# Optimization experiments

Measured on AMD Instinct MI355X. Metric: run time of the kernel, lower is better.

Reference implementation:

```python
import jax, jax.numpy as jnp
import numpy as np

EMBED_DIM = 512
NUM_HEADS = 8
HEAD_DIM = EMBED_DIM // NUM_HEADS  # 64


def setup_inputs() -> dict:
    key = jax.random.key(0)
    ks = jax.random.split(key, 11)
    B, S, E, dh = 4, 2048, EMBED_DIM, HEAD_DIM
    s_small = 1.0 / np.sqrt(dh)
    s_big = 1.0 / np.sqrt(E)
    return {
        "Q": jax.random.normal(ks[0], (B, S, E), jnp.float32),
        "K": jax.random.normal(ks[1], (B, S, E), jnp.float32),
        "V": jax.random.normal(ks[2], (B, S, E), jnp.float32),
        "Wq_w": jax.random.normal(ks[3], (dh, dh), jnp.float32) * s_small,
        "Wq_b": jnp.zeros((dh,), jnp.float32),
        "Wk_w": jax.random.normal(ks[4], (dh, dh), jnp.float32) * s_small,
        "Wk_b": jnp.zeros((dh,), jnp.float32),
        "Wv_w": jax.random.normal(ks[5], (dh, dh), jnp.float32) * s_small,
        "Wv_b": jnp.zeros((dh,), jnp.float32),
        "Wo_w": jax.random.normal(ks[6], (E, E), jnp.float32) * s_big,
        "Wo_b": jnp.zeros((E,), jnp.float32),
    }


def reference(Q, K, V, Wq_w, Wq_b, Wk_w, Wk_b, Wv_w, Wv_b, Wo_w, Wo_b):
    B, S, E = Q.shape
    H, dh = NUM_HEADS, HEAD_DIM
    # split heads: [B,S,E] -> [B,S,H,dh]; per-head shared linear (torch y = x @ W.T + b)
    q = jnp.einsum('bshd,od->bsho', Q.reshape(B, S, H, dh), Wq_w) + Wq_b
    k = jnp.einsum('bshd,od->bsho', K.reshape(B, S, H, dh), Wk_w) + Wk_b
    v = jnp.einsum('bshd,od->bsho', V.reshape(B, S, H, dh), Wv_w) + Wv_b
    # [B,H,S,dh]
    q = q.transpose(0, 2, 1, 3)
    k = k.transpose(0, 2, 1, 3)
    v = v.transpose(0, 2, 1, 3)
    scores = jnp.einsum('bhqd,bhkd->bhqk', q, k) / np.sqrt(dh)  # full N x N scores (faithful to naive impl)
    probs = jax.nn.softmax(scores, axis=-1)
    attn = jnp.einsum('bhqk,bhkd->bhqd', probs, v)
    # combine heads: [B,H,S,dh] -> [B,S,E]
    out = attn.transpose(0, 2, 1, 3).reshape(B, S, E)
    return out @ Wo_w.T + Wo_b
```

## Files before the change

### kernel.cpp

```cpp
#include <hip/hip_runtime.h>

typedef float  f32x4  __attribute__((ext_vector_type(4)));
typedef float  f32x16 __attribute__((ext_vector_type(16)));
typedef short  s16x8  __attribute__((ext_vector_type(8)));

constexpr int Bn = 4, Sn = 2048, En = 512, Hn = 8;
constexpr int BH = Bn * Hn;
constexpr int NT = Sn / 64;
constexpr float QSCL = 0.125f * 1.44269504088896f;

static __device__ __forceinline__ ushort f2bf(float f) {
  union { float f; uint u; } v; v.f = f;
  uint r = v.u + 0x7fffu + ((v.u >> 16) & 1u);
  return (ushort)(r >> 16);
}
static __device__ __forceinline__ float hexp2(float x) {
  float r; asm("v_exp_f32 %0, %1" : "=v"(r) : "v"(x)); return r;
}
static __device__ __forceinline__ uint pkbf(float lo, float hi2) {
  uint r; asm("v_cvt_pk_bf16_f32 %0, %1, %2" : "=v"(r) : "v"(lo), "v"(hi2)); return r;
}
static __device__ __forceinline__ uint2 pack4(float a, float b, float c, float d) {
  uint2 u; u.x = pkbf(a, b); u.y = pkbf(c, d); return u;
}
#define SWAP32(a, b) asm("v_permlane32_swap_b32 %0, %1" : "+v"(a), "+v"(b))
static __device__ __forceinline__ s16x8 mk8(uint a, uint b, uint c, uint d) {
  union { uint u[4]; s16x8 v; } x; x.u[0] = a; x.u[1] = b; x.u[2] = c; x.u[3] = d; return x.v;
}
#define MFMA32(A, B, C) __builtin_amdgcn_mfma_f32_32x32x16_bf16((A), (B), (C), 0, 0, 0)
#define MFMA16(A, B, C) __builtin_amdgcn_mfma_f32_16x16x32_bf16((A), (B), (C), 0, 0, 0)
#define GLDS(SRC, DST) __builtin_amdgcn_global_load_lds( \
    (const __attribute__((address_space(1))) void*)(SRC), \
    (__attribute__((address_space(3))) void*)(DST), 16, 0, 0)

__global__ __launch_bounds__(256) void proj_kernel(
    const float* __restrict__ Qi, const float* __restrict__ Ki, const float* __restrict__ Vi,
    const float* __restrict__ Wq, const float* __restrict__ bq,
    const float* __restrict__ Wk, const float* __restrict__ bk,
    const float* __restrict__ Wv, const float* __restrict__ bv,
    ushort* __restrict__ qo, ushort* __restrict__ ko, ushort* __restrict__ vto)
{
  constexpr int LP = 72;
  __shared__ ushort Xl[64 * LP];
  __shared__ ushort Wl[64 * LP];
  const int role = blockIdx.z;
  const float* X    = role == 0 ? Qi : (role == 1 ? Ki : Vi);
  const float* W    = role == 0 ? Wq : (role == 1 ? Wk : Wv);
  const float* bias = role == 0 ? bq : (role == 1 ? bk : bv);
  const float oscl  = role == 0 ? QSCL : 1.0f;
  const int t = threadIdx.x, lane = t & 63, w = t >> 6;
  const int g = lane >> 4, ql = lane & 15;
  const int bh = blockIdx.y, b = bh >> 3, h = bh & 7;
  const int s0 = blockIdx.x * 64;

  {
    const int row = t >> 4, c = t & 15;
#pragma unroll
    for (int p = 0; p < 4; ++p) {
      const int rr = row + p * 16;
      const float4 wv = *(const float4*)(W + rr * 64 + c * 4);
      *(uint2*)&Wl[rr * LP + c * 4] = pack4(wv.x, wv.y, wv.z, wv.w);
      const float4 xv = *(const float4*)(X + ((size_t)b * Sn + s0 + rr) * En + h * 64 + c * 4);
      *(uint2*)&Xl[rr * LP + c * 4] = pack4(xv.x, xv.y, xv.z, xv.w);
    }
  }
  __syncthreads();

  f32x4 acc[4];
#pragma unroll
  for (int i = 0; i < 4; ++i) acc[i] = (f32x4){0.f, 0.f, 0.f, 0.f};
#pragma unroll
  for (int kc = 0; kc < 2; ++kc) {
    const s16x8 bfrag = *(const s16x8*)&Xl[(w * 16 + ql) * LP + kc * 32 + g * 8];
#pragma unroll
    for (int nt = 0; nt < 4; ++nt) {
      const s16x8 afrag = *(const s16x8*)&Wl[(nt * 16 + ql) * LP + kc * 32 + g * 8];
      acc[nt] = MFMA16(afrag, bfrag, acc[nt]);
    }
  }

  __syncthreads();
  const int sl = w * 16 + ql;
  if (role < 2) {
#pragma unroll
    for (int nt = 0; nt < 4; ++nt) {
      const int ob = nt * 16 + g * 4;
      *(uint2*)&Xl[sl * LP + ob] = pack4((acc[nt][0] + bias[ob]) * oscl,
                                         (acc[nt][1] + bias[ob + 1]) * oscl,
                                         (acc[nt][2] + bias[ob + 2]) * oscl,
                                         (acc[nt][3] + bias[ob + 3]) * oscl);
    }
    __syncthreads();
    ushort* dst = (role == 0 ? qo : ko) + (size_t)bh * Sn * 64;
    const int ro = t >> 3, ch = t & 7;
#pragma unroll
    for (int p = 0; p < 2; ++p) {
      const int row = ro + p * 32;
      const uint4 v = *(const uint4*)&Xl[row * LP + ch * 8];
      *(uint4*)&dst[(size_t)(s0 + row) * 64 + ch * 8] = v;
    }
  } else {
#pragma unroll
    for (int nt = 0; nt < 4; ++nt)
#pragma unroll
      for (int r = 0; r < 4; ++r) {
        const int o = nt * 16 + g * 4 + r;
        Xl[o * LP + sl] = f2bf(acc[nt][r] + bias[o]);
      }
    __syncthreads();
    const int ro = t >> 3, ch = t & 7;
#pragma unroll
    for (int p = 0; p < 2; ++p) {
      const int row = ro + p * 32;
      const uint4 v = *(const uint4*)&Xl[row * LP + ch * 8];
      *(uint4*)&vto[((size_t)bh * 64 + row) * Sn + s0 + ch * 8] = v;
    }
  }
}

__global__ __launch_bounds__(512, 4) void flash_kernel(
    const ushort* __restrict__ q, const ushort* __restrict__ k,
    const ushort* __restrict__ vt, ushort* __restrict__ attn)
{
  __shared__ __align__(16) char smem[36864];
  float* mrg = (float*)smem;
  const int tid = threadIdx.x, lane = tid & 63, w = tid >> 6;
  const int m = lane & 31, hi = lane >> 5;
  const int wl = w & 3, h2 = w >> 2;
  const int hx  = hi ^ (m & 7);
  const int hxv = hx ^ (h2 << 2);

  int lid = blockIdx.x + (blockIdx.y << 4);
  lid = (lid & 7) * 64 + (lid >> 3);
  const int bq = lid & 15, bh = lid >> 4;
  const int qrow = bq * 128 + wl * 32 + m;
  const int b = bh >> 3, h = bh & 7;

  const ushort* qp = q + ((size_t)bh * Sn + qrow) * 64 + hi * 8;
  const s16x8 qf0 = *(const s16x8*)(qp + 0);
  const s16x8 qf1 = *(const s16x8*)(qp + 16);
  const s16x8 qf2 = *(const s16x8*)(qp + 32);
  const s16x8 qf3 = *(const s16x8*)(qp + 48);

  const int srow = tid >> 3, sc = tid & 7, scs = sc ^ (srow & 7);
  const ushort* kS = k  + (size_t)bh * Sn * 64 + (size_t)srow * 64 + scs * 8;
  const ushort* vS = vt + ((size_t)bh * 64 + srow) * Sn + scs * 8;
  const uint dO = (uint)(tid * 16);
  char* KB0 = smem;          char* KB1 = smem + 8192;
  char* VB0 = smem + 16384;  char* VB1 = smem + 24576;

  const f32x16 z16 = {};
  f32x16 acc0 = {}, acc1 = {}, asum = {};
  union { ushort us[8]; s16x8 v; } onesU;
#pragma unroll
  for (int i = 0; i < 8; ++i) onesU.us[i] = 0x3F80;
  const s16x8 ones = onesU.v;

  GLDS(kS, KB0 + dO); GLDS(vS, VB0 + dO);
  kS += 4096; vS += 64;

#define LDK(KB, S)     (*(const s16x8*)((KB)  + ((h2 * 32 + m) * 64 + (((2 * (S)) ^ hx ) << 3)) * 2))
#define LDV(VB, DT, S) (*(const s16x8*)((VB)  + (((DT) * 32 + m) * 64 + (((2 * (S)) ^ hxv) << 3)) * 2))

#define STEP(T, KB, VB, KBn, VBn) do {                                      \
    if ((T) < NT - 1) {                                                     \
      GLDS(kS, (KBn) + dO); GLDS(vS, (VBn) + dO);                           \
      kS += 4096; vS += 64;                                                 \
      asm volatile("s_waitcnt vmcnt(2)" ::: "memory");                      \
    } else {                                                                \
      asm volatile("s_waitcnt vmcnt(0)" ::: "memory");                      \
    }                                                                       \
    __builtin_amdgcn_s_barrier();                                           \
    __builtin_amdgcn_sched_barrier(0);                                      \
    f32x16 sta, stb;                                                        \
    __builtin_amdgcn_s_setprio(1);                                          \
    sta = MFMA32(LDK(KB, 0), qf0, z16);                                     \
    sta = MFMA32(LDK(KB, 1), qf1, sta);                                     \
    stb = MFMA32(LDK(KB, 2), qf2, z16);                                     \
    stb = MFMA32(LDK(KB, 3), qf3, stb);                                     \
    __builtin_amdgcn_s_setprio(0);                                          \
    f32x16 p;                                                               \
    _Pragma("unroll")                                                       \
    for (int i = 0; i < 16; ++i) p[i] = hexp2(sta[i] + stb[i]);             \
    uint uA, uB, uC, uD, uE, uF, uG, uH;                                    \
    uA = pkbf(p[0], p[1]);   uB = pkbf(p[4], p[5]);   SWAP32(uA, uB);       \
    uC = pkbf(p[2], p[3]);   uD = pkbf(p[6], p[7]);   SWAP32(uC, uD);       \
    uE = pkbf(p[8], p[9]);   uF = pkbf(p[12], p[13]); SWAP32(uE, uF);       \
    uG = pkbf(p[10], p[11]); uH = pkbf(p[14], p[15]); SWAP32(uG, uH);       \
    const s16x8 pb0 = mk8(uA, uC, uB, uD);                                  \
    const s16x8 pb1 = mk8(uE, uG, uF, uH);                                  \
    __builtin_amdgcn_s_setprio(1);                                          \
    acc0 = MFMA32(LDV(VB, 0, 0), pb0, acc0);                                \
    acc0 = MFMA32(LDV(VB, 0, 1), pb1, acc0);                                \
    acc1 = MFMA32(LDV(VB, 1, 0), pb0, acc1);                                \
    acc1 = MFMA32(LDV(VB, 1, 1), pb1, acc1);                                \
    asum = MFMA32(ones, pb0, asum);                                         \
    asum = MFMA32(ones, pb1, asum);                                         \
    __builtin_amdgcn_s_setprio(0);                                          \
    __builtin_amdgcn_s_barrier();                                           \
    __builtin_amdgcn_sched_barrier(0);                                      \
  } while (0)

  for (int T = 0; T < NT; T += 2) {
    STEP(T,     KB0, VB0, KB1, VB1);
    STEP(T + 1, KB1, VB1, KB0, VB0);
  }
#undef STEP
#undef LDK
#undef LDV

  const float lT = asum[0];
  float* mp = mrg + (size_t)(wl * 64 + lane) * 36;
  __syncthreads();
  if (h2) {
#pragma unroll
    for (int i = 0; i < 4; ++i) {
      f32x4 t0 = {acc0[4 * i], acc0[4 * i + 1], acc0[4 * i + 2], acc0[4 * i + 3]};
      f32x4 t1 = {acc1[4 * i], acc1[4 * i + 1], acc1[4 * i + 2], acc1[4 * i + 3]};
      *(f32x4*)(mp + 4 * i) = t0;
      *(f32x4*)(mp + 16 + 4 * i) = t1;
    }
    mp[32] = lT;
  }
  __syncthreads();
  if (!h2) {
    const float inv = 1.0f / (lT + mp[32]);
    ushort* ap = attn + ((size_t)(b * Sn + qrow)) * En + h * 64;
#pragma unroll
    for (int g2 = 0; g2 < 4; ++g2) {
      float a0 = (acc0[g2 * 4 + 0] + mp[g2 * 4 + 0]) * inv;
      float a1 = (acc0[g2 * 4 + 1] + mp[g2 * 4 + 1]) * inv;
      float a2 = (acc0[g2 * 4 + 2] + mp[g2 * 4 + 2]) * inv;
      float a3 = (acc0[g2 * 4 + 3] + mp[g2 * 4 + 3]) * inv;
      float c0 = (acc1[g2 * 4 + 0] + mp[16 + g2 * 4 + 0]) * inv;
      float c1 = (acc1[g2 * 4 + 1] + mp[16 + g2 * 4 + 1]) * inv;
      float c2 = (acc1[g2 * 4 + 2] + mp[16 + g2 * 4 + 2]) * inv;
      float c3 = (acc1[g2 * 4 + 3] + mp[16 + g2 * 4 + 3]) * inv;
      uint2 u0, u1;
      u0.x = pkbf(a0, a1); u0.y = pkbf(a2, a3);
      u1.x = pkbf(c0, c1); u1.y = pkbf(c2, c3);
      *(uint2*)&ap[g2 * 8 + hi * 4]      = u0;
      *(uint2*)&ap[32 + g2 * 8 + hi * 4] = u1;
    }
  }
}

__global__ __launch_bounds__(512) void outproj_kernel(
    const ushort* __restrict__ attn, const float* __restrict__ Wo,
    const float* __restrict__ bo, float* __restrict__ out)
{
  constexpr int LP = 72;
  __shared__ ushort Al[128 * LP];
  __shared__ ushort Wl[64 * LP];
  const int t = threadIdx.x, lane = t & 63, w = t >> 6;
  const int g = lane >> 4, ml = lane & 15;
  const int wm = w & 3, wn = w >> 2;
  const int m0 = blockIdx.x * 128, n0 = blockIdx.y * 64;
  f32x4 acc[2][2];
#pragma unroll
  for (int i = 0; i < 2; ++i)
#pragma unroll
    for (int j = 0; j < 2; ++j) acc[i][j] = (f32x4){0.f, 0.f, 0.f, 0.f};

  const int arow = t >> 2, ac0 = t & 3;
  const int wrow = t >> 3, wc0 = t & 7;
  for (int e0 = 0; e0 < En; e0 += 64) {
    __syncthreads();
#pragma unroll
    for (int p = 0; p < 2; ++p) {
      const int c = ac0 + p * 4;
      const uint4 v = *(const uint4*)(attn + ((size_t)(m0 + arow)) * En + e0 + c * 8);
      *(uint4*)&Al[arow * LP + c * 8] = v;
    }
#pragma unroll
    for (int p = 0; p < 2; ++p) {
      const int c = wc0 + p * 8;
      const float4 v = *(const float4*)(Wo + ((size_t)(n0 + wrow)) * En + e0 + c * 4);
      *(uint2*)&Wl[wrow * LP + c * 4] = pack4(v.x, v.y, v.z, v.w);
    }
    __syncthreads();
#pragma unroll
    for (int kc = 0; kc < 2; ++kc) {
      s16x8 bfr[2];
#pragma unroll
      for (int mf = 0; mf < 2; ++mf)
        bfr[mf] = *(const s16x8*)&Al[(wm * 32 + mf * 16 + ml) * LP + kc * 32 + g * 8];
#pragma unroll
      for (int nf = 0; nf < 2; ++nf) {
        const s16x8 afr = *(const s16x8*)&Wl[(wn * 32 + nf * 16 + ml) * LP + kc * 32 + g * 8];
#pragma unroll
        for (int mf = 0; mf < 2; ++mf)
          acc[mf][nf] = MFMA16(afr, bfr[mf], acc[mf][nf]);
      }
    }
  }
#pragma unroll
  for (int mf = 0; mf < 2; ++mf) {
    const int mrow = m0 + wm * 32 + mf * 16 + ml;
#pragma unroll
    for (int nf = 0; nf < 2; ++nf) {
      const int ncol = n0 + wn * 32 + nf * 16 + g * 4;
      const float4 bias = *(const float4*)(bo + ncol);
      float4 o;
      o.x = acc[mf][nf][0] + bias.x;
      o.y = acc[mf][nf][1] + bias.y;
      o.z = acc[mf][nf][2] + bias.z;
      o.w = acc[mf][nf][3] + bias.w;
      *(float4*)&out[(size_t)mrow * En + ncol] = o;
    }
  }
}

extern "C" void kernel_launch(void* const* d_in, const int* in_sizes, int n_in,
                              void* d_out, int out_size, void* d_ws, size_t ws_size,
                              hipStream_t stream) {
  const float* Qi = (const float*)d_in[0];
  const float* Ki = (const float*)d_in[1];
  const float* Vi = (const float*)d_in[2];
  const float* Wq = (const float*)d_in[3];
  const float* bq = (const float*)d_in[4];
  const float* Wk = (const float*)d_in[5];
  const float* bk = (const float*)d_in[6];
  const float* Wv = (const float*)d_in[7];
  const float* bv = (const float*)d_in[8];
  const float* Wo = (const float*)d_in[9];
  const float* bo = (const float*)d_in[10];

  const size_t TEN = (size_t)BH * Sn * 64;
  ushort* qw  = (ushort*)d_ws;
  ushort* kw  = qw + TEN;
  ushort* vtw = kw + TEN;
  ushort* at  = vtw + TEN;

  proj_kernel<<<dim3(Sn / 64, BH, 3), 256, 0, stream>>>(
      Qi, Ki, Vi, Wq, bq, Wk, bk, Wv, bv, qw, kw, vtw);
  flash_kernel<<<dim3(16, 32), 512, 0, stream>>>(qw, kw, vtw, at);
  outproj_kernel<<<dim3(Bn * Sn / 128, En / 64), 512, 0, stream>>>(
      at, Wo, bo, (float*)d_out);
}
```

Before: 76.48 us.

## Split KV sequence across two blocks and merge partials in output projection

Adds an optional two-way split of the key/value sequence in the flash kernel, so each block handles half the KV tiles and writes unnormalized bf16 partial outputs plus row sums. The output-projection kernel then adds the two partials, divides by the summed normalizers and packs the result to bf16 before the GEMM. The goal is more blocks and better load balance across CUs. The cost is twice the intermediate traffic, an extra bf16 rounding of the partials, and more combine work in the outproj loads. The split only turns on when the workspace is large enough.

```diff
diff --git a/kernel.cpp b/kernel.cpp
--- a/kernel.cpp
+++ b/kernel.cpp
@@ -7,12 +7,16 @@
 constexpr int Bn = 4, Sn = 2048, En = 512, Hn = 8;
 constexpr int BH = Bn * Hn;
 constexpr int NT = Sn / 64;
+constexpr int TENc = BH * Sn * 64;
 constexpr float QSCL = 0.125f * 1.44269504088896f;
 
 static __device__ __forceinline__ ushort f2bf(float f) {
   union { float f; uint u; } v; v.f = f;
   uint r = v.u + 0x7fffu + ((v.u >> 16) & 1u);
   return (ushort)(r >> 16);
+}
+static __device__ __forceinline__ float bf2f(uint u16) {
+  union { uint i; float f; } v; v.i = u16 << 16; return v.f;
 }
 static __device__ __forceinline__ float hexp2(float x) {
   float r; asm("v_exp_f32 %0, %1" : "=v"(r) : "v"(x)); return r;
@@ -120,7 +124,7 @@
 
 __global__ __launch_bounds__(512, 4) void flash_kernel(
     const ushort* __restrict__ q, const ushort* __restrict__ k,
-    const ushort* __restrict__ vt, ushort* __restrict__ attn)
+    const ushort* __restrict__ vt, ushort* __restrict__ accP, float* __restrict__ lP)
 {
   __shared__ __align__(16) char smem[36864];
   float* mrg = (float*)smem;
@@ -130,6 +134,10 @@
   const int hx  = hi ^ (m & 7);
   const int hxv = hx ^ (h2 << 2);
 
+  const int nz = (int)gridDim.z;
+  const int nsteps = (nz == 2) ? (NT / 2) : NT;
+  const int kvoff = (nz == 2) ? (int)blockIdx.z * (Sn / 2) : 0;
+
   int lid = blockIdx.x + (blockIdx.y << 4);
   lid = (lid & 7) * 64 + (lid >> 3);
   const int bq = lid & 15, bh = lid >> 4;
@@ -143,8 +151,8 @@
   const s16x8 qf3 = *(const s16x8*)(qp + 48);
 
   const int srow = tid >> 3, sc = tid & 7, scs = sc ^ (srow & 7);
-  const ushort* kS = k  + (size_t)bh * Sn * 64 + (size_t)srow * 64 + scs * 8;
-  const ushort* vS = vt + ((size_t)bh * 64 + srow) * Sn + scs * 8;
+  const ushort* kS = k  + (size_t)bh * Sn * 64 + (size_t)(kvoff + srow) * 64 + scs * 8;
+  const ushort* vS = vt + ((size_t)bh * 64 + srow) * Sn + kvoff + scs * 8;
   const uint dO = (uint)(tid * 16);
   char* KB0 = smem;          char* KB1 = smem + 8192;
   char* VB0 = smem + 16384;  char* VB1 = smem + 24576;
@@ -163,7 +171,7 @@
 #define LDV(VB, DT, S) (*(const s16x8*)((VB)  + (((DT) * 32 + m) * 64 + (((2 * (S)) ^ hxv) << 3)) * 2))
 
 #define STEP(T, KB, VB, KBn, VBn) do {                                      \
-    if ((T) < NT - 1) {                                                     \
+    if ((T) < nsteps - 1) {                                                 \
       GLDS(kS, (KBn) + dO); GLDS(vS, (VBn) + dO);                           \
       kS += 4096; vS += 64;                                                 \
       asm volatile("s_waitcnt vmcnt(2)" ::: "memory");                      \
@@ -201,7 +209,7 @@
     __builtin_amdgcn_sched_barrier(0);                                      \
   } while (0)
 
-  for (int T = 0; T < NT; T += 2) {
+  for (int T = 0; T < nsteps; T += 2) {
     STEP(T,     KB0, VB0, KB1, VB1);
     STEP(T + 1, KB1, VB1, KB0, VB0);
   }
@@ -224,18 +232,21 @@
   }
   __syncthreads();
   if (!h2) {
-    const float inv = 1.0f / (lT + mp[32]);
-    ushort* ap = attn + ((size_t)(b * Sn + qrow)) * En + h * 64;
+    const float lTot = lT + mp[32];
+    const float sc = (nz == 1) ? (1.0f / lTot) : 1.0f;
+    if (nz == 2 && hi == 0)
+      lP[((size_t)blockIdx.z * (Bn * Sn) + b * Sn + qrow) * Hn + h] = lTot;
+    ushort* ap = accP + ((size_t)blockIdx.z * TENc) + ((size_t)(b * Sn + qrow)) * En + h * 64;
 #pragma unroll
     for (int g2 = 0; g2 < 4; ++g2) {
-      float a0 = (acc0[g2 * 4 + 0] + mp[g2 * 4 + 0]) * inv;
-      float a1 = (acc0[g2 * 4 + 1] + mp[g2 * 4 + 1]) * inv;
-      float a2 = (acc0[g2 * 4 + 2] + mp[g2 * 4 + 2]) * inv;
-      float a3 = (acc0[g2 * 4 + 3] + mp[g2 * 4 + 3]) * inv;
-      float c0 = (acc1[g2 * 4 + 0] + mp[16 + g2 * 4 + 0]) * inv;
-      float c1 = (acc1[g2 * 4 + 1] + mp[16 + g2 * 4 + 1]) * inv;
-      float c2 = (acc1[g2 * 4 + 2] + mp[16 + g2 * 4 + 2]) * inv;
-      float c3 = (acc1[g2 * 4 + 3] + mp[16 + g2 * 4 + 3]) * inv;
+      float a0 = (acc0[g2 * 4 + 0] + mp[g2 * 4 + 0]) * sc;
+      float a1 = (acc0[g2 * 4 + 1] + mp[g2 * 4 + 1]) * sc;
+      float a2 = (acc0[g2 * 4 + 2] + mp[g2 * 4 + 2]) * sc;
+      float a3 = (acc0[g2 * 4 + 3] + mp[g2 * 4 + 3]) * sc;
+      float c0 = (acc1[g2 * 4 + 0] + mp[16 + g2 * 4 + 0]) * sc;
+      float c1 = (acc1[g2 * 4 + 1] + mp[16 + g2 * 4 + 1]) * sc;
+      float c2 = (acc1[g2 * 4 + 2] + mp[16 + g2 * 4 + 2]) * sc;
+      float c3 = (acc1[g2 * 4 + 3] + mp[16 + g2 * 4 + 3]) * sc;
       uint2 u0, u1;
       u0.x = pkbf(a0, a1); u0.y = pkbf(a2, a3);
       u1.x = pkbf(c0, c1); u1.y = pkbf(c2, c3);
@@ -246,8 +257,8 @@
 }
 
 __global__ __launch_bounds__(512) void outproj_kernel(
-    const ushort* __restrict__ attn, const float* __restrict__ Wo,
-    const float* __restrict__ bo, float* __restrict__ out)
+    const ushort* __restrict__ accP, const float* __restrict__ lP, const int nz,
+    const float* __restrict__ Wo, const float* __restrict__ bo, float* __restrict__ out)
 {
   constexpr int LP = 72;
   __shared__ ushort Al[128 * LP];
@@ -264,13 +275,40 @@
 
   const int arow = t >> 2, ac0 = t & 3;
   const int wrow = t >> 3, wc0 = t & 7;
+  const int mr = m0 + arow;
+
   for (int e0 = 0; e0 < En; e0 += 64) {
     __syncthreads();
-#pragma unroll
-    for (int p = 0; p < 2; ++p) {
-      const int c = ac0 + p * 4;
-      const uint4 v = *(const uint4*)(attn + ((size_t)(m0 + arow)) * En + e0 + c * 8);
-      *(uint4*)&Al[arow * LP + c * 8] = v;
+    if (nz == 1) {
+#pragma unroll
+      for (int p = 0; p < 2; ++p) {
+        const int c = ac0 + p * 4;
+        const uint4 u = *(const uint4*)(accP + (size_t)mr * En + e0 + c * 8);
+        *(uint4*)&Al[arow * LP + c * 8] = u;
+      }
+    } else {
+      const int hh = e0 >> 6;
+      const float invl = 1.0f / (lP[(size_t)mr * Hn + hh] +
+                                 lP[((size_t)(Bn * Sn) + mr) * Hn + hh]);
+#pragma unroll
+      for (int p = 0; p < 2; ++p) {
+        const int c = ac0 + p * 4;
+        const size_t off = (size_t)mr * En + e0 + c * 8;
+        const uint4 u = *(const uint4*)(accP + off);
+        const uint4 v2 = *(const uint4*)(accP + (size_t)TENc + off);
+        float s0 = bf2f(u.x & 0xffff) + bf2f(v2.x & 0xffff);
+        float s1 = bf2f(u.x >> 16)    + bf2f(v2.x >> 16);
+        float s2 = bf2f(u.y & 0xffff) + bf2f(v2.y & 0xffff);
+        float s3 = bf2f(u.y >> 16)    + bf2f(v2.y >> 16);
+        float s4 = bf2f(u.z & 0xffff) + bf2f(v2.z & 0xffff);
+        float s5 = bf2f(u.z >> 16)    + bf2f(v2.z >> 16);
+        float s6 = bf2f(u.w & 0xffff) + bf2f(v2.w & 0xffff);
+        float s7 = bf2f(u.w >> 16)    + bf2f(v2.w >> 16);
+        uint4 o;
+        o.x = pkbf(s0 * invl, s1 * invl); o.y = pkbf(s2 * invl, s3 * invl);
+        o.z = pkbf(s4 * invl, s5 * invl); o.w = pkbf(s6 * invl, s7 * invl);
+        *(uint4*)&Al[arow * LP + c * 8] = o;
+      }
     }
 #pragma unroll
     for (int p = 0; p < 2; ++p) {
@@ -326,15 +364,18 @@
   const float* Wo = (const float*)d_in[9];
   const float* bo = (const float*)d_in[10];
 
-  const size_t TEN = (size_t)BH * Sn * 64;
-  ushort* qw  = (ushort*)d_ws;
-  ushort* kw  = qw + TEN;
-  ushort* vtw = kw + TEN;
-  ushort* at  = vtw + TEN;
+  const size_t TEN = (size_t)TENc;
+  ushort* qw   = (ushort*)d_ws;
+  ushort* kw   = qw + TEN;
+  ushort* vtw  = kw + TEN;
+  ushort* accP = vtw + TEN;
+
+  const int nz = (ws_size >= (size_t)42467328) ? 2 : 1;
+  float* lP = (float*)(accP + (size_t)nz * TEN);
 
   proj_kernel<<<dim3(Sn / 64, BH, 3), 256, 0, stream>>>(
       Qi, Ki, Vi, Wq, bq, Wk, bk, Wv, bv, qw, kw, vtw);
-  flash_kernel<<<dim3(16, 32), 512, 0, stream>>>(qw, kw, vtw, at);
+  flash_kernel<<<dim3(16, 32, nz), 512, 0, stream>>>(qw, kw, vtw, accP, lP);
   outproj_kernel<<<dim3(Bn * Sn / 128, En / 64), 512, 0, stream>>>(
-      at, Wo, bo, (float*)d_out);
-}
+      accP, lP, nz, Wo, bo, (float*)d_out);
+}
```

Result: slower. 83.13 us (+8.7%).
